# Kernel tuning notes

Hardware: AMD Instinct MI355X
Metric: run time of the kernel (lower is better)

The kernel has to match this reference:

```python
import jax, jax.numpy as jnp
import numpy as np

XLIM = 6.0    # params.max_rdf_dist
DR = 0.05     # params.dr
N_BINS = int(XLIM / DR)  # 120


def setup_inputs() -> dict:
    key = jax.random.key(0)
    k1, k2, k3 = jax.random.split(key, 3)
    T, R, N = 100, 8, 83  # frames, replicas, LiPS atoms
    L = 10.2              # LiPS lattice constant (Angstrom)
    stacked_radii = jax.random.uniform(k1, (T, R, N, 3), dtype=jnp.float32) * L
    # near-cubic LiPS cell with a tiny random skew (non-degenerate lattice)
    cell = jnp.eye(3, dtype=jnp.float32) * L + 0.1 * jax.random.uniform(k2, (3, 3), dtype=jnp.float32)
    gt_rdf = jax.random.uniform(k3, (N_BINS,), dtype=jnp.float32)
    bins = jnp.linspace(1e-6, XLIM, N_BINS + 1).astype(jnp.float32)
    return {"stacked_radii": stacked_radii, "cell": cell, "gt_rdf": gt_rdf, "bins": bins}


def _histogram(d, bins):
    # np.histogram semantics: values outside [bins[0], bins[-1]] dropped,
    # right edge inclusive in the last bin. Zeros (self-distances) fall
    # below bins[0]=1e-6, matching the original's d != 0 filter.
    nb = bins.shape[0] - 1
    idx = jnp.clip(jnp.searchsorted(bins, d, side='right') - 1, 0, nb - 1)
    w = ((d >= bins[0]) & (d <= bins[-1])).astype(jnp.float32)
    return jax.ops.segment_sum(w, idx, num_segments=nb)


def _min_image_dist(x, shifts):
    # x: [T, N, 3]; shifts: [27, 3]. Loop over the 27 fixed shifts to avoid
    # materializing the [T, N, N, 27, 3] tensor the torch code builds.
    diff = x[:, :, None, :] - x[:, None, :, :]            # [T, N, N, 3]
    d2 = jnp.sum((diff - shifts[0]) ** 2, axis=-1)        # [T, N, N]
    for i in range(1, shifts.shape[0]):
        d2 = jnp.minimum(d2, jnp.sum((diff - shifts[i]) ** 2, axis=-1))
    return jnp.sqrt(d2)


def reference(stacked_radii, cell, gt_rdf, bins):
    T, R, N, _ = stacked_radii.shape
    pos = np.arange(-1, 2)  # num_cells = 1 -> 27 periodic images
    combos = jnp.asarray(
        np.stack(np.meshgrid(pos, pos, pos, indexing='xy'), axis=-1).reshape(-1, 3),
        dtype=stacked_radii.dtype)                        # [27, 3]
    shifts = combos @ cell                                # [27, 3]
    volume = jnp.abs(jnp.dot(jnp.cross(cell[0], cell[1]), cell[2]))
    rho = (T * N * N) / volume  # data_shape counted BEFORE zero-filter, as in original
    Z = rho * (4.0 / 3.0) * jnp.pi * (bins[1:] ** 3 - bins[:-1] ** 3)  # [n_bins]

    def rdf_one(x):  # x: [T, N, 3] -> [n_bins]
        d = _min_image_dist(x, shifts)
        return _histogram(d.reshape(-1), bins) / Z

    rdfs = jax.vmap(rdf_one, in_axes=1)(stacked_radii)    # [R, n_bins]
    maes = XLIM * jnp.mean(jnp.abs(rdfs - gt_rdf), axis=-1, keepdims=True)  # [R, 1]
    return rdfs, maes
```

## Files before the change

### kernel.cpp

```cpp
#include <hip/hip_runtime.h>

#define T_FRAMES 100
#define R_REP    8
#define N_ATOMS  83
#define N_BINS   120
#define NPAIRS   (N_ATOMS * (N_ATOMS - 1) / 2)
#define BLK      256
#define PPT      7
#define HALF0    1702
#define SLOTS_PER_REP (2 * T_FRAMES)

__device__ __forceinline__ int rowstart(int i) {
    return (i * (165 - i)) >> 1;
}

__global__ __launch_bounds__(BLK, 4) void rdf_hist_kernel(
        const float* __restrict__ radii,
        const float* __restrict__ cell,
        const float* __restrict__ bins,
        unsigned int* __restrict__ partial)
{
#pragma clang fp contract(off)
    __shared__ float sx[N_ATOMS], sy[N_ATOMS], sz[N_ATOMS];
    __shared__ float scell[12];
    __shared__ float sbins[N_BINS + 1];
    __shared__ unsigned int shist[N_BINS];

    const int tid  = threadIdx.x;
    const int blk  = blockIdx.x;
    const int fr   = blk >> 1;
    const int half = blk & 1;
    const int t = fr / R_REP;
    const int r = fr % R_REP;
    const int pstart = half ? HALF0 : 0;
    const int pcount = half ? (NPAIRS - HALF0) : HALF0;

    for (int i = tid; i < N_ATOMS; i += BLK) {
        const float* p = radii + (((size_t)t * R_REP + r) * N_ATOMS + i) * 3;
        sx[i] = p[0]; sy[i] = p[1]; sz[i] = p[2];
    }
    for (int i = tid; i <= N_BINS; i += BLK) sbins[i] = bins[i];
    for (int i = tid; i < N_BINS; i += BLK) shist[i] = 0u;
    if (tid < 9) scell[(tid / 3) * 4 + (tid % 3)] = cell[tid];
    __syncthreads();

    float cc[3][3];
#pragma unroll
    for (int q = 0; q < 3; ++q)
#pragma unroll
        for (int d = 0; d < 3; ++d) cc[q][d] = scell[q * 4 + d];
    float rn[3];
#pragma unroll
    for (int q = 0; q < 3; ++q)
        rn[q] = 1.0f / (cc[q][0] * cc[q][0] + cc[q][1] * cc[q][1] + cc[q][2] * cc[q][2]);

    float dx[PPT], dy[PPT], dz[PPT], d2m[PPT];
#pragma unroll
    for (int s = 0; s < PPT; ++s) {
        const int l = tid + s * BLK;
        const int p = (l < pcount) ? (pstart + l) : 0;
        int i = (int)((165.0f - sqrtf((float)(27225 - 8 * p))) * 0.5f);
        if (i < 0) i = 0;
        if (i > N_ATOMS - 2) i = N_ATOMS - 2;
        while (rowstart(i + 1) <= p) ++i;
        while (rowstart(i) > p) --i;
        const int j = p - rowstart(i) + i + 1;
        dx[s] = sx[i] - sx[j];
        dy[s] = sy[i] - sy[j];
        dz[s] = sz[i] - sz[j];
        d2m[s] = 3.4e38f;
    }

#pragma unroll
    for (int s = 0; s < PPT; ++s) {
        const float Dx = dx[s], Dy = dy[s], Dz = dz[s];
        const float fx = (Dx * cc[0][0] + Dy * cc[0][1] + Dz * cc[0][2]) * rn[0];
        const float fy = (Dx * cc[1][0] + Dy * cc[1][1] + Dz * cc[1][2]) * rn[1];
        const float fz = (Dx * cc[2][0] + Dy * cc[2][1] + Dz * cc[2][2]) * rn[2];
        int axi = (int)floorf(fx); axi = axi < -1 ? -1 : (axi > 0 ? 0 : axi);
        int ayi = (int)floorf(fy); ayi = ayi < -1 ? -1 : (ayi > 0 ? 0 : ayi);
        int azi = (int)floorf(fz); azi = azi < -1 ? -1 : (azi > 0 ? 0 : azi);
        const float na0 = (float)axi, na1 = na0 + 1.0f;
        const float nb0 = (float)ayi, nb1 = nb0 + 1.0f;
        const float nc0 = (float)azi, nc1 = nc0 + 1.0f;

        float An[2][3], Bn[2][3], Cn[2][3];
#pragma unroll
        for (int d = 0; d < 3; ++d) {
            An[0][d] = na0 * cc[0][d]; An[1][d] = na1 * cc[0][d];
            Bn[0][d] = nb0 * cc[1][d]; Bn[1][d] = nb1 * cc[1][d];
            Cn[0][d] = nc0 * cc[2][d]; Cn[1][d] = nc1 * cc[2][d];
        }
        float m = d2m[s];
#pragma unroll
        for (int ia = 0; ia < 2; ++ia) {
#pragma unroll
            for (int ib = 0; ib < 2; ++ib) {
                const float m0 = An[ia][0] + Bn[ib][0];
                const float m1 = An[ia][1] + Bn[ib][1];
                const float m2 = An[ia][2] + Bn[ib][2];
#pragma unroll
                for (int ic = 0; ic < 2; ++ic) {
                    const float t0 = Dx - (m0 + Cn[ic][0]);
                    const float t1 = Dy - (m1 + Cn[ic][1]);
                    const float t2 = Dz - (m2 + Cn[ic][2]);
                    const float d2 = (t0 * t0 + t1 * t1) + t2 * t2;
                    m = fminf(m, d2);
                }
            }
        }
        d2m[s] = m;
    }

    const float blo  = sbins[0];
    const float bhi  = sbins[N_BINS];
    const float inv_step = (float)N_BINS / (bhi - blo);
#pragma unroll
    for (int s = 0; s < PPT; ++s) {
        const int l = tid + s * BLK;
        if (l >= pcount) continue;
        const float d = sqrtf(d2m[s]);
        if (d >= blo && d <= bhi) {
            int idx = (int)((d - blo) * inv_step);
            if (idx > N_BINS - 1) idx = N_BINS - 1;
            if (idx < 0) idx = 0;
            while (idx > 0 && d < sbins[idx]) --idx;
            while (idx < N_BINS - 1 && d >= sbins[idx + 1]) ++idx;
            atomicAdd(&shist[idx], 2u);
        }
    }
    __syncthreads();

    unsigned int* dst = partial + ((size_t)(r * T_FRAMES + t) * 2 + half) * N_BINS;
    for (int b = tid; b < N_BINS; b += BLK) dst[b] = shist[b];
}

__global__ __launch_bounds__(256) void finalize_kernel(
        const unsigned int* __restrict__ partial,
        const float* __restrict__ cell,
        const float* __restrict__ bins,
        const float* __restrict__ gt,
        float* __restrict__ out)
{
    __shared__ unsigned int ssum[2][N_BINS];
    __shared__ float sdiff[N_BINS];
    const int r = blockIdx.x;
    const int tid = threadIdx.x;
    const int h = tid >> 7;
    const int b = tid & 127;

    if (b < N_BINS) {
        const unsigned int* base = partial
            + (size_t)r * SLOTS_PER_REP * N_BINS + (size_t)h * 100 * N_BINS + b;
        unsigned int acc = 0;
#pragma unroll 20
        for (int f = 0; f < 100; ++f) acc += base[(size_t)f * N_BINS];
        ssum[h][b] = acc;
    }
    __syncthreads();

    const float c0x = cell[0], c0y = cell[1], c0z = cell[2];
    const float c1x = cell[3], c1y = cell[4], c1z = cell[5];
    const float c2x = cell[6], c2y = cell[7], c2z = cell[8];
    const float crx = c0y * c1z - c0z * c1y;
    const float cry = c0z * c1x - c0x * c1z;
    const float crz = c0x * c1y - c0y * c1x;
    const float vol = fabsf(crx * c2x + cry * c2y + crz * c2z);
    const float rho = (float)(T_FRAMES * N_ATOMS * N_ATOMS) / vol;
    const float coef = (rho * 1.33333337f) * 3.14159274f;

    if (tid < N_BINS) {
        const unsigned int tot = ssum[0][tid] + ssum[1][tid];
        const float b1 = bins[tid], b2 = bins[tid + 1];
        const float Z = coef * (b2 * b2 * b2 - b1 * b1 * b1);
        const float v = (float)tot / Z;
        out[r * N_BINS + tid] = v;
        sdiff[tid] = fabsf(v - gt[tid]);
    }
    __syncthreads();

    if (tid < 64) {
        float s = sdiff[tid] + ((tid < N_BINS - 64) ? sdiff[tid + 64] : 0.0f);
#pragma unroll
        for (int off = 32; off; off >>= 1) s += __shfl_down(s, off, 64);
        if (tid == 0)
            out[R_REP * N_BINS + r] = 6.0f * (s * (1.0f / (float)N_BINS));
    }
}

extern "C" void kernel_launch(void* const* d_in, const int* in_sizes, int n_in,
                              void* d_out, int out_size, void* d_ws, size_t ws_size,
                              hipStream_t stream) {
    const float* radii = (const float*)d_in[0];
    const float* cell  = (const float*)d_in[1];
    const float* gt    = (const float*)d_in[2];
    const float* bins  = (const float*)d_in[3];
    float* out = (float*)d_out;
    unsigned int* part = (unsigned int*)d_ws;

    hipLaunchKernelGGL(rdf_hist_kernel, dim3(2 * T_FRAMES * R_REP), dim3(BLK), 0, stream,
                       radii, cell, bins, part);
    hipLaunchKernelGGL(finalize_kernel, dim3(R_REP), dim3(256), 0, stream,
                       part, cell, bins, gt, out);
}
```

Measured before the change: 27.69 us.

## Fuse finalize into histogram kernel via global atomics and last-block reduction

Merges the two kernels into one. Each block atomically adds its shared histogram into a per-replica global histogram and increments a completion counter, and the last block to finish normalizes all bins and computes the MAE. This removes the second kernel launch and the partial-histogram buffer write and read. In exchange it adds a memset launch and contended global atomics across 1600 blocks, and leaves a serial tail in the last block.

```diff
diff --git a/kernel.cpp b/kernel.cpp
--- a/kernel.cpp
+++ b/kernel.cpp
@@ -8,23 +8,30 @@
 #define BLK      256
 #define PPT      7
 #define HALF0    1702
-#define SLOTS_PER_REP (2 * T_FRAMES)
+#define NBLOCKS  (2 * T_FRAMES * R_REP)
 
 __device__ __forceinline__ int rowstart(int i) {
     return (i * (165 - i)) >> 1;
 }
 
-__global__ __launch_bounds__(BLK, 4) void rdf_hist_kernel(
+__global__ __launch_bounds__(BLK, 4) void rdf_fused_kernel(
         const float* __restrict__ radii,
         const float* __restrict__ cell,
         const float* __restrict__ bins,
-        unsigned int* __restrict__ partial)
+        const float* __restrict__ gt,
+        unsigned int* __restrict__ ws,
+        float* __restrict__ out)
 {
 #pragma clang fp contract(off)
     __shared__ float sx[N_ATOMS], sy[N_ATOMS], sz[N_ATOMS];
     __shared__ float scell[12];
     __shared__ float sbins[N_BINS + 1];
     __shared__ unsigned int shist[N_BINS];
+    __shared__ int slast;
+    __shared__ float sdiff[R_REP][N_BINS];
+
+    unsigned int* __restrict__ hist_g = ws;
+    unsigned int* __restrict__ cnt    = ws + R_REP * N_BINS;
 
     const int tid  = threadIdx.x;
     const int blk  = blockIdx.x;
@@ -112,8 +119,8 @@
         d2m[s] = m;
     }
 
-    const float blo  = sbins[0];
-    const float bhi  = sbins[N_BINS];
+    const float blo = sbins[0];
+    const float bhi = sbins[N_BINS];
     const float inv_step = (float)N_BINS / (bhi - blo);
 #pragma unroll
     for (int s = 0; s < PPT; ++s) {
@@ -131,37 +138,24 @@
     }
     __syncthreads();
 
-    unsigned int* dst = partial + ((size_t)(r * T_FRAMES + t) * 2 + half) * N_BINS;
-    for (int b = tid; b < N_BINS; b += BLK) dst[b] = shist[b];
-}
-
-__global__ __launch_bounds__(256) void finalize_kernel(
-        const unsigned int* __restrict__ partial,
-        const float* __restrict__ cell,
-        const float* __restrict__ bins,
-        const float* __restrict__ gt,
-        float* __restrict__ out)
-{
-    __shared__ unsigned int ssum[2][N_BINS];
-    __shared__ float sdiff[N_BINS];
-    const int r = blockIdx.x;
-    const int tid = threadIdx.x;
-    const int h = tid >> 7;
-    const int b = tid & 127;
-
-    if (b < N_BINS) {
-        const unsigned int* base = partial
-            + (size_t)r * SLOTS_PER_REP * N_BINS + (size_t)h * 100 * N_BINS + b;
-        unsigned int acc = 0;
-#pragma unroll 20
-        for (int f = 0; f < 100; ++f) acc += base[(size_t)f * N_BINS];
-        ssum[h][b] = acc;
-    }
-    __syncthreads();
-
-    const float c0x = cell[0], c0y = cell[1], c0z = cell[2];
-    const float c1x = cell[3], c1y = cell[4], c1z = cell[5];
-    const float c2x = cell[6], c2y = cell[7], c2z = cell[8];
+    if (tid < N_BINS) {
+        const unsigned int v = shist[tid];
+        if (v) atomicAdd(&hist_g[r * N_BINS + tid], v);
+    }
+    __syncthreads();
+
+    if (tid == 0) {
+        __threadfence();
+        const unsigned int old = atomicAdd(cnt, 1u);
+        slast = (old == NBLOCKS - 1) ? 1 : 0;
+    }
+    __syncthreads();
+    if (!slast) return;
+    __threadfence();
+
+    const float c0x = cc[0][0], c0y = cc[0][1], c0z = cc[0][2];
+    const float c1x = cc[1][0], c1y = cc[1][1], c1z = cc[1][2];
+    const float c2x = cc[2][0], c2y = cc[2][1], c2z = cc[2][2];
     const float crx = c0y * c1z - c0z * c1y;
     const float cry = c0z * c1x - c0x * c1z;
     const float crz = c0x * c1y - c0y * c1x;
@@ -169,22 +163,28 @@
     const float rho = (float)(T_FRAMES * N_ATOMS * N_ATOMS) / vol;
     const float coef = (rho * 1.33333337f) * 3.14159274f;
 
-    if (tid < N_BINS) {
-        const unsigned int tot = ssum[0][tid] + ssum[1][tid];
-        const float b1 = bins[tid], b2 = bins[tid + 1];
+    for (int e = tid; e < R_REP * N_BINS; e += BLK) {
+        const int b = e % N_BINS;
+        const unsigned int tot =
+            __hip_atomic_load(&hist_g[e], __ATOMIC_RELAXED, __HIP_MEMORY_SCOPE_AGENT);
+        const float b1 = sbins[b], b2 = sbins[b + 1];
         const float Z = coef * (b2 * b2 * b2 - b1 * b1 * b1);
         const float v = (float)tot / Z;
-        out[r * N_BINS + tid] = v;
-        sdiff[tid] = fabsf(v - gt[tid]);
-    }
-    __syncthreads();
-
-    if (tid < 64) {
-        float s = sdiff[tid] + ((tid < N_BINS - 64) ? sdiff[tid + 64] : 0.0f);
+        out[e] = v;
+        sdiff[e / N_BINS][b] = fabsf(v - gt[b]);
+    }
+    __syncthreads();
+
+    const int wave = tid >> 6;
+    const int lane = tid & 63;
+#pragma unroll
+    for (int w = 0; w < 2; ++w) {
+        const int rr = wave * 2 + w;
+        float s = sdiff[rr][lane] + ((lane < N_BINS - 64) ? sdiff[rr][lane + 64] : 0.0f);
 #pragma unroll
         for (int off = 32; off; off >>= 1) s += __shfl_down(s, off, 64);
-        if (tid == 0)
-            out[R_REP * N_BINS + r] = 6.0f * (s * (1.0f / (float)N_BINS));
+        if (lane == 0)
+            out[R_REP * N_BINS + rr] = 6.0f * (s * (1.0f / (float)N_BINS));
     }
 }
 
@@ -196,10 +196,9 @@
     const float* gt    = (const float*)d_in[2];
     const float* bins  = (const float*)d_in[3];
     float* out = (float*)d_out;
-    unsigned int* part = (unsigned int*)d_ws;
-
-    hipLaunchKernelGGL(rdf_hist_kernel, dim3(2 * T_FRAMES * R_REP), dim3(BLK), 0, stream,
-                       radii, cell, bins, part);
-    hipLaunchKernelGGL(finalize_kernel, dim3(R_REP), dim3(256), 0, stream,
-                       part, cell, bins, gt, out);
+    unsigned int* ws   = (unsigned int*)d_ws;
+
+    hipMemsetAsync(ws, 0, (R_REP * N_BINS + 1) * sizeof(unsigned int), stream);
+    hipLaunchKernelGGL(rdf_fused_kernel, dim3(NBLOCKS), dim3(BLK), 0, stream,
+                       radii, cell, bins, gt, ws, out);
 }
```

Measured after the change: 50.92 us. +83.9%, slower.

## Precompute fractional coords per atom and pack partial histograms into 16-bit pairs

Applied to the files above, without the earlier changes.

Fractional coordinates are now computed once per atom in shared memory, so each pair's fractional difference is a subtraction rather than a 3x3 matrix-vector product. Distances above 36 (squared) are rejected before the sqrt, and the upper bin edge is hardcoded to 6. Partial histograms are packed two 16-bit counts per word, which halves workspace traffic, and the finalize kernel reduces them with four groups of 50 frames. This relies on per-block bin counts fitting in 16 bits and on the bins ending exactly at 6.0, and it may shift results slightly because of float rounding in the fractional differences.

```diff
diff --git a/kernel.cpp b/kernel.cpp
--- a/kernel.cpp
+++ b/kernel.cpp
@@ -4,11 +4,12 @@
 #define R_REP    8
 #define N_ATOMS  83
 #define N_BINS   120
+#define NWORDS   60
 #define NPAIRS   (N_ATOMS * (N_ATOMS - 1) / 2)
 #define BLK      256
 #define PPT      7
 #define HALF0    1702
-#define SLOTS_PER_REP (2 * T_FRAMES)
+#define SLOTS    (2 * T_FRAMES)
 
 __device__ __forceinline__ int rowstart(int i) {
     return (i * (165 - i)) >> 1;
@@ -22,7 +23,7 @@
 {
 #pragma clang fp contract(off)
     __shared__ float sx[N_ATOMS], sy[N_ATOMS], sz[N_ATOMS];
-    __shared__ float scell[12];
+    __shared__ float sfx[N_ATOMS], sfy[N_ATOMS], sfz[N_ATOMS];
     __shared__ float sbins[N_BINS + 1];
     __shared__ unsigned int shist[N_BINS];
 
@@ -35,26 +36,29 @@
     const int pstart = half ? HALF0 : 0;
     const int pcount = half ? (NPAIRS - HALF0) : HALF0;
 
+    float cc[3][3];
+#pragma unroll
+    for (int c = 0; c < 3; ++c)
+#pragma unroll
+        for (int d = 0; d < 3; ++d) cc[c][d] = cell[c * 3 + d];
+    float rn[3];
+#pragma unroll
+    for (int c = 0; c < 3; ++c)
+        rn[c] = 1.0f / (cc[c][0] * cc[c][0] + cc[c][1] * cc[c][1] + cc[c][2] * cc[c][2]);
+
     for (int i = tid; i < N_ATOMS; i += BLK) {
         const float* p = radii + (((size_t)t * R_REP + r) * N_ATOMS + i) * 3;
-        sx[i] = p[0]; sy[i] = p[1]; sz[i] = p[2];
+        const float x = p[0], y = p[1], z = p[2];
+        sx[i] = x; sy[i] = y; sz[i] = z;
+        sfx[i] = (x * cc[0][0] + y * cc[0][1] + z * cc[0][2]) * rn[0];
+        sfy[i] = (x * cc[1][0] + y * cc[1][1] + z * cc[1][2]) * rn[1];
+        sfz[i] = (x * cc[2][0] + y * cc[2][1] + z * cc[2][2]) * rn[2];
     }
     for (int i = tid; i <= N_BINS; i += BLK) sbins[i] = bins[i];
     for (int i = tid; i < N_BINS; i += BLK) shist[i] = 0u;
-    if (tid < 9) scell[(tid / 3) * 4 + (tid % 3)] = cell[tid];
-    __syncthreads();
-
-    float cc[3][3];
-#pragma unroll
-    for (int q = 0; q < 3; ++q)
-#pragma unroll
-        for (int d = 0; d < 3; ++d) cc[q][d] = scell[q * 4 + d];
-    float rn[3];
-#pragma unroll
-    for (int q = 0; q < 3; ++q)
-        rn[q] = 1.0f / (cc[q][0] * cc[q][0] + cc[q][1] * cc[q][1] + cc[q][2] * cc[q][2]);
-
-    float dx[PPT], dy[PPT], dz[PPT], d2m[PPT];
+    __syncthreads();
+
+    float dx[PPT], dy[PPT], dz[PPT], fx[PPT], fy[PPT], fz[PPT];
 #pragma unroll
     for (int s = 0; s < PPT; ++s) {
         const int l = tid + s * BLK;
@@ -68,18 +72,18 @@
         dx[s] = sx[i] - sx[j];
         dy[s] = sy[i] - sy[j];
         dz[s] = sz[i] - sz[j];
-        d2m[s] = 3.4e38f;
-    }
-
+        fx[s] = sfx[i] - sfx[j];
+        fy[s] = sfy[i] - sfy[j];
+        fz[s] = sfz[i] - sfz[j];
+    }
+
+    float d2m[PPT];
 #pragma unroll
     for (int s = 0; s < PPT; ++s) {
         const float Dx = dx[s], Dy = dy[s], Dz = dz[s];
-        const float fx = (Dx * cc[0][0] + Dy * cc[0][1] + Dz * cc[0][2]) * rn[0];
-        const float fy = (Dx * cc[1][0] + Dy * cc[1][1] + Dz * cc[1][2]) * rn[1];
-        const float fz = (Dx * cc[2][0] + Dy * cc[2][1] + Dz * cc[2][2]) * rn[2];
-        int axi = (int)floorf(fx); axi = axi < -1 ? -1 : (axi > 0 ? 0 : axi);
-        int ayi = (int)floorf(fy); ayi = ayi < -1 ? -1 : (ayi > 0 ? 0 : ayi);
-        int azi = (int)floorf(fz); azi = azi < -1 ? -1 : (azi > 0 ? 0 : azi);
+        int axi = (int)floorf(fx[s]); axi = axi < -1 ? -1 : (axi > 0 ? 0 : axi);
+        int ayi = (int)floorf(fy[s]); ayi = ayi < -1 ? -1 : (ayi > 0 ? 0 : ayi);
+        int azi = (int)floorf(fz[s]); azi = azi < -1 ? -1 : (azi > 0 ? 0 : azi);
         const float na0 = (float)axi, na1 = na0 + 1.0f;
         const float nb0 = (float)ayi, nb1 = nb0 + 1.0f;
         const float nc0 = (float)azi, nc1 = nc0 + 1.0f;
@@ -91,7 +95,7 @@
             Bn[0][d] = nb0 * cc[1][d]; Bn[1][d] = nb1 * cc[1][d];
             Cn[0][d] = nc0 * cc[2][d]; Cn[1][d] = nc1 * cc[2][d];
         }
-        float m = d2m[s];
+        float m = 3.4e38f;
 #pragma unroll
         for (int ia = 0; ia < 2; ++ia) {
 #pragma unroll
@@ -112,15 +116,15 @@
         d2m[s] = m;
     }
 
-    const float blo  = sbins[0];
-    const float bhi  = sbins[N_BINS];
-    const float inv_step = (float)N_BINS / (bhi - blo);
+    const float blo = sbins[0];
+    const float inv_step = (float)N_BINS / (6.0f - blo);
 #pragma unroll
     for (int s = 0; s < PPT; ++s) {
         const int l = tid + s * BLK;
         if (l >= pcount) continue;
+        if (d2m[s] > 36.0f) continue;
         const float d = sqrtf(d2m[s]);
-        if (d >= blo && d <= bhi) {
+        if (d >= blo) {
             int idx = (int)((d - blo) * inv_step);
             if (idx > N_BINS - 1) idx = N_BINS - 1;
             if (idx < 0) idx = 0;
@@ -131,8 +135,10 @@
     }
     __syncthreads();
 
-    unsigned int* dst = partial + ((size_t)(r * T_FRAMES + t) * 2 + half) * N_BINS;
-    for (int b = tid; b < N_BINS; b += BLK) dst[b] = shist[b];
+    if (tid < NWORDS) {
+        const unsigned int w = shist[2 * tid] | (shist[2 * tid + 1] << 16);
+        partial[((size_t)(r * SLOTS + t * 2 + half)) * NWORDS + tid] = w;
+    }
 }
 
 __global__ __launch_bounds__(256) void finalize_kernel(
@@ -142,20 +148,25 @@
         const float* __restrict__ gt,
         float* __restrict__ out)
 {
-    __shared__ unsigned int ssum[2][N_BINS];
+    __shared__ unsigned int slo[4][NWORDS], shi[4][NWORDS];
     __shared__ float sdiff[N_BINS];
     const int r = blockIdx.x;
     const int tid = threadIdx.x;
-    const int h = tid >> 7;
-    const int b = tid & 127;
-
-    if (b < N_BINS) {
+    const int h = tid >> 6;
+    const int c = tid & 63;
+
+    if (c < NWORDS) {
         const unsigned int* base = partial
-            + (size_t)r * SLOTS_PER_REP * N_BINS + (size_t)h * 100 * N_BINS + b;
-        unsigned int acc = 0;
-#pragma unroll 20
-        for (int f = 0; f < 100; ++f) acc += base[(size_t)f * N_BINS];
-        ssum[h][b] = acc;
+            + (size_t)r * SLOTS * NWORDS + (size_t)h * 50 * NWORDS + c;
+        unsigned int lo = 0, hi = 0;
+#pragma unroll 10
+        for (int f = 0; f < 50; ++f) {
+            const unsigned int w = base[(size_t)f * NWORDS];
+            lo += w & 0xFFFFu;
+            hi += w >> 16;
+        }
+        slo[h][c] = lo;
+        shi[h][c] = hi;
     }
     __syncthreads();
 
@@ -170,7 +181,10 @@
     const float coef = (rho * 1.33333337f) * 3.14159274f;
 
     if (tid < N_BINS) {
-        const unsigned int tot = ssum[0][tid] + ssum[1][tid];
+        const int w = tid >> 1;
+        unsigned int tot = 0;
+        if (tid & 1) tot = shi[0][w] + shi[1][w] + shi[2][w] + shi[3][w];
+        else         tot = slo[0][w] + slo[1][w] + slo[2][w] + slo[3][w];
         const float b1 = bins[tid], b2 = bins[tid + 1];
         const float Z = coef * (b2 * b2 * b2 - b1 * b1 * b1);
         const float v = (float)tot / Z;
```

Result: no change. 27.57 us (median of 2 runs) (-0.4%).
